# Optimization experiments

Measured on AMD Instinct MI355X. Metric: run time of the kernel, lower is better.

The kernel has to match this reference:

```python
import jax, jax.numpy as jnp
import numpy as np
from jax import lax

B, TZ, TT = 16, 2048, 512
D, DFF, L, V, HEADS = 256, 1024, 6, 512, 4
CH, HID, K, FLOWS, G = 256, 256, 5, 4, 256
PAD_ID = 0
NEG = -1e9
SCALE = 0.02


def setup_inputs():
    key = jax.random.key(0)
    ks = jax.random.split(key, 20)
    n = lambda i, shape, s=SCALE: jax.random.normal(ks[i], shape, jnp.float32) * s
    return {
        'z': jax.random.normal(ks[0], (B, TZ, CH), jnp.float32),
        'text': jax.random.randint(ks[1], (B, TT), 1, V),  # low=1 so no pad tokens
        'cond': jax.random.normal(ks[2], (B, G), jnp.float32),
        'embed': n(3, (V, D), 1.0),
        'wq': n(4, (L, D, D)), 'wk': n(5, (L, D, D)), 'wv': n(6, (L, D, D)), 'wo': n(7, (L, D, D)),
        'bq': jnp.zeros((L, D)), 'bk': jnp.zeros((L, D)), 'bv': jnp.zeros((L, D)), 'bo': jnp.zeros((L, D)),
        'ln1_g': jnp.ones((L, D)), 'ln1_b': jnp.zeros((L, D)),
        'ln2_g': jnp.ones((L, D)), 'ln2_b': jnp.zeros((L, D)),
        'w1': n(8, (L, D, DFF)), 'b1': jnp.zeros((L, DFF)),
        'w2': n(9, (L, DFF, D)), 'b2': jnp.zeros((L, D)),
        'mu_w': n(10, (D, D)), 'mu_b': jnp.zeros((D,)),
        'lv_w': n(11, (D, D)), 'lv_b': jnp.zeros((D,)),
        'flow_in': n(12, (FLOWS, CH // 2, HID)), 'flow_in_b': jnp.zeros((FLOWS, HID)),
        'flow_cond': n(13, (FLOWS, G, HID)),
        'flow_conv': n(14, (FLOWS, K, HID, HID)), 'flow_conv_b': jnp.zeros((FLOWS, HID)),
        'flow_out': n(15, (FLOWS, HID, CH // 2)), 'flow_out_b': jnp.zeros((FLOWS, CH // 2)),
    }


def _pos_encoding(length, d):
    pos = np.arange(length)[:, None].astype(np.float32)
    i = np.arange(d)[None, :]
    angle = pos / np.power(10000.0, (2 * (i // 2)) / d)
    pe = np.where(i % 2 == 0, np.sin(angle), np.cos(angle))
    return jnp.asarray(pe, jnp.float32)


def _ln(x, g, b):
    m = jnp.mean(x, -1, keepdims=True)
    v = jnp.var(x, -1, keepdims=True)
    return g * (x - m) * lax.rsqrt(v + 1e-6) + b


def _mha(x, wq, wk, wv, wo, bq, bk, bv, bo, bias):
    Bq, T, _ = x.shape
    dh = D // HEADS
    heads = lambda y: y.reshape(Bq, T, HEADS, dh).transpose(0, 2, 1, 3)
    q, k, v = heads(x @ wq + bq), heads(x @ wk + bk), heads(x @ wv + bv)
    scores = jnp.einsum('bhqd,bhkd->bhqk', q, k) / jnp.sqrt(jnp.float32(dh)) + bias
    attn = jax.nn.softmax(scores, axis=-1)
    out = jnp.einsum('bhqk,bhkd->bhqd', attn, v).transpose(0, 2, 1, 3).reshape(Bq, T, D)
    return out @ wo + bo


def _mas_path(logp, text_mask):
    # Viterbi monotonic alignment: each latent frame t maps to text index j(t),
    # j nondecreasing with steps in {0, 1}, start at 0, end at last valid token.
    Bq, Tz, Tt = logp.shape
    Q0 = jnp.where(jnp.arange(Tt) == 0, logp[:, 0, :], NEG)

    def fwd(Q, lt):
        Qs = jnp.concatenate([jnp.full((Bq, 1), NEG, Q.dtype), Q[:, :-1]], axis=1)
        return lt + jnp.maximum(Q, Qs), Qs > Q  # choice True => came from j-1

    _, choices = lax.scan(fwd, Q0, jnp.swapaxes(logp, 0, 1)[1:])  # [Tz-1,B,Tt]
    j_last = jnp.sum(text_mask, axis=1).astype(jnp.int32) - 1

    def bwd(j, ch):
        c = jnp.take_along_axis(ch, j[:, None], axis=1)[:, 0]
        jp = j - c.astype(jnp.int32)
        return jp, jp

    _, path_rev = lax.scan(bwd, j_last, choices[::-1])
    path = jnp.concatenate([path_rev[::-1], j_last[None]], axis=0)  # [Tz,B]
    return jnp.swapaxes(path, 0, 1)


def _forward(z, text, cond, embed, wq, wk, wv, wo, bq, bk, bv, bo, ln1_g, ln1_b, ln2_g, ln2_b,
             w1, b1, w2, b2, mu_w, mu_b, lv_w, lv_b,
             flow_in, flow_in_b, flow_cond, flow_conv, flow_conv_b, flow_out, flow_out_b):
    text_mask = text != PAD_ID  # [B,TT]
    bias = jnp.where(text_mask[:, None, None, :], 0.0, NEG)
    # text encoder: scaled embedding + sinusoidal PE + post-LN transformer blocks
    h = embed[text] * jnp.sqrt(jnp.float32(D)) + _pos_encoding(TT, D)[None]
    for l in range(L):
        h = _ln(h + _mha(h, wq[l], wk[l], wv[l], wo[l], bq[l], bk[l], bv[l], bo[l], bias), ln1_g[l], ln1_b[l])
        ffn = jax.nn.relu(h @ w1[l] + b1[l]) @ w2[l] + b2[l]
        h = _ln(h + ffn, ln2_g[l], ln2_b[l])
    mu = h @ mu_w + mu_b
    logvar = h @ lv_w + lv_b
    # residual coupling flows (mean-only, conditioned on global vector)
    zc = z
    for f in range(FLOWS):
        x0, x1 = jnp.split(zc, 2, axis=-1)
        hh = x0 @ flow_in[f] + flow_in_b[f] + (cond @ flow_cond[f])[:, None, :]
        hh = jnp.tanh(lax.conv_general_dilated(hh, flow_conv[f], (1,), 'SAME', rhs_dilation=(1,),
                                               dimension_numbers=('NWC', 'WIO', 'NWC')) + flow_conv_b[f])
        m = hh @ flow_out[f] + flow_out_b[f]
        zc = jnp.concatenate([x1 + m, x0], axis=-1)  # coupling + flip
    # gaussian log-likelihood between latent frames and text distributions
    spr = jnp.exp(-logvar)  # [B,TT,D]
    nc1 = jnp.sum(-0.5 * jnp.log(2.0 * jnp.pi) - 0.5 * logvar, axis=-1)  # [B,TT]
    nc2 = jnp.einsum('btd,bjd->btj', -0.5 * zc * zc, spr)
    nc3 = jnp.einsum('btd,bjd->btj', zc, mu * spr)
    nc4 = jnp.sum(-0.5 * mu * mu * spr, axis=-1)  # [B,TT]
    logp = nc1[:, None, :] + nc2 + nc3 + nc4[:, None, :]  # [B,TZ,TT]
    logp = jnp.where(text_mask[:, None, :], logp, NEG)
    path = _mas_path(logp, text_mask)  # [B,TZ] int32
    ctx = mu[jnp.arange(B)[:, None], path]  # expand text mu along latent time
    return ctx, h


def reference(z, text, cond, embed, wq, wk, wv, wo, bq, bk, bv, bo, ln1_g, ln1_b, ln2_g, ln2_b,
              w1, b1, w2, b2, mu_w, mu_b, lv_w, lv_b,
              flow_in, flow_in_b, flow_cond, flow_conv, flow_conv_b, flow_out, flow_out_b):
    return _forward(z, text, cond, embed, wq, wk, wv, wo, bq, bk, bv, bo, ln1_g, ln1_b, ln2_g, ln2_b,
                    w1, b1, w2, b2, mu_w, mu_b, lv_w, lv_b,
                    flow_in, flow_in_b, flow_cond, flow_conv, flow_conv_b, flow_out, flow_out_b)
```

## Files before the change

kernel.cpp:

```cpp
#include <hip/hip_runtime.h>

#define BB 16
#define TZ_ 2048
#define TT_ 512
#define D_ 256
#define DFF_ 1024
#define L_ 6
#define HEADS_ 4
#define DH_ 64
#define CH_ 256
#define HID_ 256
#define KCV 5
#define FLOWS_ 4
#define G_ 256
#define NEGF (-1000000000.0f)
#define LOG2PI 1.8378770664093453f

typedef unsigned short u16;
typedef __attribute__((ext_vector_type(8))) short short8v;
typedef __attribute__((ext_vector_type(4))) float f32x4;
typedef __attribute__((ext_vector_type(4))) unsigned u4v;

__device__ __forceinline__ float wsum(float v){
#pragma unroll
  for (int o = 32; o; o >>= 1) v += __shfl_xor(v, o);
  return v;
}
__device__ __forceinline__ u16 f2bf(float x){
  unsigned u = __float_as_uint(x);
  return (u16)((u + 0x7FFFu + ((u >> 16) & 1u)) >> 16);
}
__device__ __forceinline__ float bf2f(u16 h){
  return __uint_as_float(((unsigned)h) << 16);
}
__device__ __forceinline__ unsigned pk2f(float a, float b){
  return __builtin_amdgcn_perm(__float_as_uint(b), __float_as_uint(a), 0x07060302u);
}
__device__ __forceinline__ float trnc(float f){
  return __uint_as_float(__float_as_uint(f) & 0xFFFF0000u);
}
__device__ __forceinline__ void cvt8t(float4 x, float4 y, uint4 &hi, uint4 &lo){
  hi.x = pk2f(x.x, x.y); hi.y = pk2f(x.z, x.w);
  hi.z = pk2f(y.x, y.y); hi.w = pk2f(y.z, y.w);
  float r0 = x.x - trnc(x.x), r1 = x.y - trnc(x.y), r2 = x.z - trnc(x.z), r3 = x.w - trnc(x.w);
  float r4 = y.x - trnc(y.x), r5 = y.y - trnc(y.y), r6 = y.z - trnc(y.z), r7 = y.w - trnc(y.w);
  lo.x = pk2f(r0, r1); lo.y = pk2f(r2, r3); lo.z = pk2f(r4, r5); lo.w = pk2f(r6, r7);
}
__device__ __forceinline__ unsigned rneh(float f){
  unsigned v = __float_as_uint(f);
  return (v + 0x7FFFu + ((v >> 16) & 1u)) & 0xFFFF0000u;
}
__device__ __forceinline__ void cvt8r(float4 x, float4 y, uint4 &hi, uint4 &lo){
  unsigned h0=rneh(x.x), h1=rneh(x.y), h2=rneh(x.z), h3=rneh(x.w);
  unsigned h4=rneh(y.x), h5=rneh(y.y), h6=rneh(y.z), h7=rneh(y.w);
  hi.x = h1 | (h0>>16); hi.y = h3 | (h2>>16); hi.z = h5 | (h4>>16); hi.w = h7 | (h6>>16);
  float r0 = x.x - __uint_as_float(h0), r1 = x.y - __uint_as_float(h1);
  float r2 = x.z - __uint_as_float(h2), r3 = x.w - __uint_as_float(h3);
  float r4 = y.x - __uint_as_float(h4), r5 = y.y - __uint_as_float(h5);
  float r6 = y.z - __uint_as_float(h6), r7 = y.w - __uint_as_float(h7);
  lo.x = pk2f(r0, r1); lo.y = pk2f(r2, r3); lo.z = pk2f(r4, r5); lo.w = pk2f(r6, r7);
}

__global__ void k_pe(float* __restrict__ pe){
  int t = blockIdx.x, d = threadIdx.x;
  double e = (double)(2*(d>>1)) / (double)D_;
  double ang = (double)t * pow(10000.0, -e);
  pe[t*D_ + d] = (float)(((d&1)==0) ? sin(ang) : cos(ang));
}
__global__ void k_embed(const int* __restrict__ text, const float* __restrict__ emb,
                        const float* __restrict__ pe, float* __restrict__ h){
  int row = blockIdx.x, d = threadIdx.x;
  h[(size_t)row*D_ + d] = emb[(size_t)text[row]*D_ + d]*16.0f + pe[(row%TT_)*D_ + d];
}

__global__ __launch_bounds__(256) void k_wt(
  const float* __restrict__ wq, const float* __restrict__ wk,
  const float* __restrict__ wv, const float* __restrict__ wo,
  const float* __restrict__ mu_w, const float* __restrict__ lv_w,
  const float* __restrict__ w1, const float* __restrict__ w2,
  float* __restrict__ QKVT, float* __restrict__ OT, float* __restrict__ MULVT,
  float* __restrict__ W1T, float* __restrict__ W2T)
{
  __shared__ float td[64][65];
  const int s = blockIdx.y, tile = blockIdx.x, t = threadIdx.x;
  const float* inb; float* outb; int istride, ostride;
  if (s < 24){
    int l = s>>2, wsel = s&3;
    const float* w = (wsel==0?wq:wsel==1?wk:wsel==2?wv:wo);
    inb = w + (size_t)l*65536; istride = 256;
    if (wsel < 3) outb = QKVT + (size_t)l*196608 + wsel*65536;
    else          outb = OT   + (size_t)l*65536;
    ostride = 256;
  } else if (s < 26){
    inb = (s==24 ? mu_w : lv_w); istride = 256;
    outb = MULVT + (size_t)(s-24)*65536; ostride = 256;
  } else if (s < 50){
    int idx = s-26, l = idx>>2, b2 = idx&3;
    inb = w1 + (size_t)l*262144 + b2*256; istride = 1024;
    outb = W1T + (size_t)l*262144 + (size_t)b2*65536; ostride = 256;
  } else {
    int idx = s-50, l = idx>>2, b2 = idx&3;
    inb = w2 + (size_t)l*262144 + (size_t)b2*65536; istride = 256;
    outb = W2T + (size_t)l*262144 + b2*256; ostride = 1024;
  }
  const int kt = (tile>>2)*64, nt = (tile&3)*64;
  const int r = t>>2, cq = (t&3)*16;
#pragma unroll
  for (int c=0;c<16;c+=4){
    float4 v = *(const float4*)(inb + (size_t)(kt + r)*istride + nt + cq + c);
    td[r][cq+c+0]=v.x; td[r][cq+c+1]=v.y; td[r][cq+c+2]=v.z; td[r][cq+c+3]=v.w;
  }
  __syncthreads();
#pragma unroll
  for (int c=0;c<16;c+=4){
    float4 v = make_float4(td[cq+c+0][r], td[cq+c+1][r], td[cq+c+2][r], td[cq+c+3][r]);
    *(float4*)(outb + (size_t)(nt + r)*ostride + kt + cq + c) = v;
  }
}

__global__ __launch_bounds__(256) void k_vt(const float* __restrict__ QKV, float* __restrict__ VT){
  __shared__ float td[64][65];
  const int b = blockIdx.z, dt = blockIdx.x, jt = blockIdx.y, t = threadIdx.x;
  const float* inb = QKV + (size_t)b*512*768 + 512;
  float* outb = VT + (size_t)b*131072;
  const int r = t>>2, cq = (t&3)*16;
#pragma unroll
  for (int c=0;c<16;c+=4){
    float4 v = *(const float4*)(inb + (size_t)(jt*64 + r)*768 + dt*64 + cq + c);
    td[r][cq+c+0]=v.x; td[r][cq+c+1]=v.y; td[r][cq+c+2]=v.z; td[r][cq+c+3]=v.w;
  }
  __syncthreads();
#pragma unroll
  for (int c=0;c<16;c+=4){
    float4 v = make_float4(td[cq+c+0][r], td[cq+c+1][r], td[cq+c+2][r], td[cq+c+3][r]);
    *(float4*)(outb + (size_t)(dt*64 + r)*512 + jt*64 + cq + c) = v;
  }
}

__global__ void k_bcat(const float* __restrict__ bq, const float* __restrict__ bk,
                       const float* __restrict__ bv, const float* __restrict__ mu_b,
                       const float* __restrict__ lv_b,
                       float* __restrict__ BQKV, float* __restrict__ MULVB){
  int i = blockIdx.x*256 + threadIdx.x;
  if (i < 4608){
    int l = i/768, c = i%768;
    float v = c<256 ? bq[l*256+c] : (c<512 ? bk[l*256+c-256] : bv[l*256+c-512]);
    BQKV[i] = v;
  } else if (i < 5120){
    int c = i-4608;
    MULVB[c] = c<256 ? mu_b[c] : lv_b[c-256];
  }
}

template<int WN, int EPI, int AM, int BMD>
__global__ __launch_bounds__(256,2) void k_mg(
  const void* __restrict__ Ap, const void* __restrict__ ApL, int lda, int azhi, int azlo,
  const void* __restrict__ Bp, const void* __restrict__ BpL, int ldb, int bzhi, int bzlo,
  const float* __restrict__ bias, const int* __restrict__ text,
  const float* __restrict__ nc1v, const float* __restrict__ nc4v,
  float* __restrict__ C, int ldc, int czhi, int czlo, int K)
{
  constexpr int BN = WN*32;
  __shared__ u16 AH[4096], AL[4096];
  __shared__ u16 BH[BN*32], BL[BN*32];
  char* AHB=(char*)AH; char* ALB=(char*)AL; char* BHB=(char*)BH; char* BLB=(char*)BL;
  const int t = threadIdx.x, z = blockIdx.z;
  const int m0 = blockIdx.y*128, n0 = blockIdx.x*BN;
  const size_t aoff = (size_t)(z>>2)*azhi + (size_t)(z&3)*azlo;
  const size_t boff = (size_t)(z>>2)*bzhi + (size_t)(z&3)*bzlo;
  const size_t coff = (size_t)(z>>2)*czhi + (size_t)(z&3)*czlo;
  const int w = t>>6, l = t&63;
  const int wr = (w>>1)*64, wc = (w&1)*(WN*16);
  const int lr = l&15, lg = l>>4;
  const int srow = t>>1, sseg = t&1;
  const int q  = (srow>>1)&3;
  const int wo0 = srow*64 + ((((sseg<<1)|0)^q)<<4);
  const int wo1 = srow*64 + ((((sseg<<1)|1)^q)<<4);
  const bool bact = (WN==4) || (t < 128);
  const int qa = ((wr+lr)>>1)&3, qb2 = ((wc+lr)>>1)&3;
  const int raBase = (wr+lr)*64 + ((lg^qa)<<4);
  const int rbBase = (wc+lr)*64 + ((lg^qb2)<<4);

  const float* Af = nullptr; const u16* AfH = nullptr; const u16* AfL = nullptr;
  if constexpr (AM==0 || AM==2 || AM==4){ Af = (const float*)Ap + aoff; }
  else { AfH = (const u16*)Ap + aoff; AfL = (const u16*)ApL + aoff; }
  const float* Bf = nullptr; const u16* BfH = nullptr; const u16* BfL = nullptr;
  if constexpr (BMD==0){ Bf = (const float*)Bp + boff; }
  else { BfH = (const u16*)Bp + boff; BfL = (const u16*)BpL + boff; }

  float mrow = 0.f, sinv = 0.f;
  if constexpr (AM==4){
    int rg = z*TT_ + m0 + srow;
    mrow = nc1v[rg];
    sinv = nc4v[rg];
  }

  float4 sa0, sa1, sa2, sa3;
  uint4  pah0, pah1, pal0, pal1;
  float4 sb0, sb1, sb2, sb3;
  uint4  pbh0, pbh1, pbl0, pbl1;

  auto LOADA = [&](int kk){
    if constexpr (AM==0 || AM==4){
      const float* p = Af + (size_t)(m0+srow)*lda + kk + sseg*16;
      sa0=*(const float4*)p; sa1=*(const float4*)(p+4);
      sa2=*(const float4*)(p+8); sa3=*(const float4*)(p+12);
    } else if constexpr (AM==1){
      const u16* ph = AfH + (size_t)(m0+srow)*lda + kk + sseg*16;
      const u16* pl = AfL + (size_t)(m0+srow)*lda + kk + sseg*16;
      pah0 = *(const uint4*)ph; pah1 = *(const uint4*)(ph+8);
      pal0 = *(const uint4*)pl; pal1 = *(const uint4*)(pl+8);
    } else {
      int kg = kk + sseg*16;
      const float* p = Af + (size_t)(m0+srow)*lda + (kg < 256 ? kg : kg - 256);
      sa0=*(const float4*)p; sa1=*(const float4*)(p+4);
      sa2=*(const float4*)(p+8); sa3=*(const float4*)(p+12);
    }
  };
  auto LOADB = [&](int kk){
    if constexpr (BMD==0){
      const float* p = Bf + (size_t)(n0+srow)*ldb + kk + sseg*16;
      sb0=*(const float4*)p; sb1=*(const float4*)(p+4);
      sb2=*(const float4*)(p+8); sb3=*(const float4*)(p+12);
    } else {
      const u16* ph = BfH + (size_t)(n0+srow)*ldb + kk + sseg*16;
      const u16* pl = BfL + (size_t)(n0+srow)*ldb + kk + sseg*16;
      pbh0 = *(const uint4*)ph; pbh1 = *(const uint4*)(ph+8);
      pbl0 = *(const uint4*)pl; pbl1 = *(const uint4*)(pl+8);
    }
  };
  auto WRITEA = [&](int kk){
    uint4 ahi0, ahi1, alo0, alo1;
    if constexpr (AM==0){
      cvt8t(sa0,sa1,ahi0,alo0); cvt8t(sa2,sa3,ahi1,alo1);
    } else if constexpr (AM==4){
      float4 a0=sa0, a1=sa1, a2=sa2, a3=sa3;
      a0.x=expf(a0.x-mrow)*sinv; a0.y=expf(a0.y-mrow)*sinv; a0.z=expf(a0.z-mrow)*sinv; a0.w=expf(a0.w-mrow)*sinv;
      a1.x=expf(a1.x-mrow)*sinv; a1.y=expf(a1.y-mrow)*sinv; a1.z=expf(a1.z-mrow)*sinv; a1.w=expf(a1.w-mrow)*sinv;
      a2.x=expf(a2.x-mrow)*sinv; a2.y=expf(a2.y-mrow)*sinv; a2.z=expf(a2.z-mrow)*sinv; a2.w=expf(a2.w-mrow)*sinv;
      a3.x=expf(a3.x-mrow)*sinv; a3.y=expf(a3.y-mrow)*sinv; a3.z=expf(a3.z-mrow)*sinv; a3.w=expf(a3.w-mrow)*sinv;
      cvt8t(a0,a1,ahi0,alo0); cvt8t(a2,a3,ahi1,alo1);
    } else if constexpr (AM==1){
      ahi0=pah0; ahi1=pah1; alo0=pal0; alo1=pal1;
    } else {
      float4 a0=sa0, a1=sa1, a2=sa2, a3=sa3;
      int kg = kk + sseg*16;
      if (kg >= 256){
        a0.x=-0.5f*a0.x*a0.x; a0.y=-0.5f*a0.y*a0.y; a0.z=-0.5f*a0.z*a0.z; a0.w=-0.5f*a0.w*a0.w;
        a1.x=-0.5f*a1.x*a1.x; a1.y=-0.5f*a1.y*a1.y; a1.z=-0.5f*a1.z*a1.z; a1.w=-0.5f*a1.w*a1.w;
        a2.x=-0.5f*a2.x*a2.x; a2.y=-0.5f*a2.y*a2.y; a2.z=-0.5f*a2.z*a2.z; a2.w=-0.5f*a2.w*a2.w;
        a3.x=-0.5f*a3.x*a3.x; a3.y=-0.5f*a3.y*a3.y; a3.z=-0.5f*a3.z*a3.z; a3.w=-0.5f*a3.w*a3.w;
      }
      cvt8r(a0,a1,ahi0,alo0); cvt8r(a2,a3,ahi1,alo1);
    }
    *(uint4*)(AHB + wo0) = ahi0;  *(uint4*)(AHB + wo1) = ahi1;
    *(uint4*)(ALB + wo0) = alo0;  *(uint4*)(ALB + wo1) = alo1;
  };
  auto WRITEB = [&](){
    uint4 bhi0, bhi1, blo0, blo1;
    if constexpr (BMD==0){
      cvt8t(sb0,sb1,bhi0,blo0); cvt8t(sb2,sb3,bhi1,blo1);
    } else {
      bhi0=pbh0; bhi1=pbh1; blo0=pbl0; blo1=pbl1;
    }
    *(uint4*)(BHB + wo0) = bhi0;  *(uint4*)(BHB + wo1) = bhi1;
    *(uint4*)(BLB + wo0) = blo0;  *(uint4*)(BLB + wo1) = blo1;
  };

  f32x4 acc[4][WN];
#pragma unroll
  for (int i=0;i<4;i++)
#pragma unroll
    for (int j=0;j<WN;j++) acc[i][j] = (f32x4){0.f,0.f,0.f,0.f};

  LOADA(0);
  if (bact) LOADB(0);
  for (int k0 = 0; k0 < K; k0 += 32){
    __syncthreads();
    WRITEA(k0);
    if (bact) WRITEB();
    if (k0 + 32 < K){ LOADA(k0+32); if (bact) LOADB(k0+32); }
    __syncthreads();
    short8v fah[4], fal[4], fbh[WN], fbl[WN];
#pragma unroll
    for (int i=0;i<4;i++){
      fah[i] = *(short8v*)(AHB + raBase + i*1024);
      fal[i] = *(short8v*)(ALB + raBase + i*1024);
    }
#pragma unroll
    for (int j=0;j<WN;j++){
      fbh[j] = *(short8v*)(BHB + rbBase + j*1024);
      fbl[j] = *(short8v*)(BLB + rbBase + j*1024);
    }
#pragma unroll
    for (int i=0;i<4;i++)
#pragma unroll
      for (int j=0;j<WN;j++){
        acc[i][j] = __builtin_amdgcn_mfma_f32_16x16x32_bf16(fah[i], fbh[j], acc[i][j], 0,0,0);
        acc[i][j] = __builtin_amdgcn_mfma_f32_16x16x32_bf16(fal[i], fbh[j], acc[i][j], 0,0,0);
        acc[i][j] = __builtin_amdgcn_mfma_f32_16x16x32_bf16(fah[i], fbl[j], acc[i][j], 0,0,0);
      }
  }

#pragma unroll
  for (int i=0;i<4;i++){
    int mm0 = m0 + wr + i*16 + (lg<<2);
#pragma unroll
    for (int j=0;j<WN;j++){
      int nn = n0 + wc + j*16 + lr;
      float bs = 0.f; float ncb = 0.f; bool msk = true;
      if (EPI==0 || EPI==1) bs = bias ? bias[nn] : 0.f;
      if (EPI==2) msk = (text[(z>>2)*TT_ + nn] != 0);
      if (EPI==3){ ncb = nc1v[z*TT_+nn] + nc4v[z*TT_+nn]; msk = (text[z*TT_+nn] != 0); }
      f32x4 v = acc[i][j];
#pragma unroll
      for (int r=0;r<4;r++){
        int m = mm0 + r;
        float x;
        if (EPI==0)      x = v[r] + bs;
        else if (EPI==1) x = fmaxf(v[r] + bs, 0.f);
        else if (EPI==2) x = v[r]*0.125f + (msk ? 0.f : NEGF);
        else             x = msk ? (v[r] + ncb) : NEGF;
        C[coff + (size_t)m*ldc + nn] = x;
      }
    }
  }
}

__global__ __launch_bounds__(256) void k_rowstat(const float* __restrict__ S,
  float* __restrict__ MR, float* __restrict__ SR){
  size_t row = (size_t)blockIdx.x*4 + (threadIdx.x >> 6);
  const float* p = S + row*TT_;
  int ln = threadIdx.x & 63;
  float4 a = *(const float4*)(p + ln*8);
  float4 b = *(const float4*)(p + ln*8 + 4);
  float x[8] = {a.x,a.y,a.z,a.w,b.x,b.y,b.z,b.w};
  float m = x[0];
#pragma unroll
  for (int i=1;i<8;i++) m = fmaxf(m, x[i]);
#pragma unroll
  for (int o2=32;o2;o2>>=1) m = fmaxf(m, __shfl_xor(m, o2));
  float s = 0.f;
#pragma unroll
  for (int i=0;i<8;i++){ s += expf(x[i]-m); }
  s = wsum(s);
  if (ln == 0){
    MR[row] = m;
    SR[row] = 1.0f/s;
  }
}

__global__ __launch_bounds__(256) void k_lnres(const float* __restrict__ y,
  const float* __restrict__ g, const float* __restrict__ bb, float* __restrict__ h){
  size_t row = blockIdx.x; int d = threadIdx.x;
  float v = h[row*D_ + d] + y[row*D_ + d];
  float s = wsum(v), s2 = wsum(v*v);
  __shared__ float r1[4], r2[4];
  int w = d >> 6;
  if ((d & 63) == 0){ r1[w] = s; r2[w] = s2; }
  __syncthreads();
  s  = r1[0]+r1[1]+r1[2]+r1[3];
  s2 = r2[0]+r2[1]+r2[2]+r2[3];
  float mean = s * (1.0f/D_);
  float var  = s2 * (1.0f/D_) - mean*mean;
  float inv  = rsqrtf(var + 1e-6f);
  h[row*D_ + d] = g[d]*(v - mean)*inv + bb[d];
}

__global__ __launch_bounds__(256) void k_prep(const float* __restrict__ mulv,
  u16* __restrict__ b2h, u16* __restrict__ b2l,
  float* __restrict__ nc1, float* __restrict__ nc4){
  size_t row = blockIdx.x; int d = threadIdx.x;
  float m = mulv[row*512 + d];
  float lv = mulv[row*512 + 256 + d];
  float sp = expf(-lv);
  float ms = m*sp;
  float s1 = wsum(lv), s2 = wsum(m*ms);
  __shared__ float r1[4], r2[4];
  int w = d >> 6;
  if ((d&63)==0){ r1[w]=s1; r2[w]=s2; }
  __syncthreads();
  if (d == 0){
    nc1[row] = -0.5f*((float)D_*LOG2PI + (r1[0]+r1[1]+r1[2]+r1[3]));
    nc4[row] = -0.5f*(r2[0]+r2[1]+r2[2]+r2[3]);
  }
  unsigned hm = rneh(ms);
  b2h[row*512 + d] = (u16)(hm>>16);
  b2l[row*512 + d] = f2bf(ms - __uint_as_float(hm));
  unsigned hs = rneh(sp);
  b2h[row*512 + 256 + d] = (u16)(hs>>16);
  b2l[row*512 + 256 + d] = f2bf(sp - __uint_as_float(hs));
}

__global__ __launch_bounds__(256) void k_fprep(
  const float* __restrict__ win, const float* __restrict__ wconv, const float* __restrict__ wout,
  u16* __restrict__ WITH, u16* __restrict__ WITL,
  u16* __restrict__ WCTH, u16* __restrict__ WCTL,
  u16* __restrict__ WOTH, u16* __restrict__ WOTL,
  const float* __restrict__ zsrc, u16* __restrict__ xh, u16* __restrict__ xl,
  const float* __restrict__ cond, const float* __restrict__ fcw, float* __restrict__ condp)
{
  const int bid = blockIdx.x, t = threadIdx.x;
  if (bid < 1536){
    int i = bid*256 + t;
    float wv2; u16 *dh, *dl; int idx;
    if (i < 32768){
      int n = i >> 7, k = i & 127;
      wv2 = win[k*256 + n]; dh = WITH; dl = WITL; idx = i;
    } else if (i < 360448){
      int jj = i - 32768;
      int o = jj / 1280, r = jj - o*1280;
      wv2 = wconv[(size_t)r*256 + o]; dh = WCTH; dl = WCTL; idx = jj;
    } else {
      int jj = i - 360448;
      int o = jj >> 8, k = jj & 255;
      wv2 = wout[k*128 + o]; dh = WOTH; dl = WOTL; idx = jj;
    }
    u16 hh = f2bf(wv2);
    dh[idx] = hh;
    dl[idx] = f2bf(wv2 - bf2f(hh));
  } else if (bid < 3584){
    size_t i = ((size_t)(bid-1536)*256 + t) << 3;
    size_t m2 = i >> 7; int k = (int)(i & 127);
    const float* src = zsrc + m2*256 + k;
    float4 a = *(const float4*)src; float4 b2 = *(const float4*)(src+4);
    float vv[8] = {a.x,a.y,a.z,a.w,b2.x,b2.y,b2.z,b2.w};
    short8v oh, ol;
#pragma unroll
    for (int r=0;r<8;r++){
      u16 hh = f2bf(vv[r]);
      oh[r] = (short)hh;
      ol[r] = (short)f2bf(vv[r] - bf2f(hh));
    }
    *(short8v*)(xh + i) = oh;
    *(short8v*)(xl + i) = ol;
  } else {
    int b = bid - 3584, n = t;
    float s = 0.f;
    for (int k2=0;k2<G_;k2++) s = fmaf(cond[b*G_ + k2], fcw[k2*HID_ + n], s);
    condp[b*HID_ + n] = s;
  }
}

__global__ void k_padzero2(u16* __restrict__ XpH, u16* __restrict__ XpL){
  int i = blockIdx.x*256 + threadIdx.x;
  u16* P = (i >> 14) ? XpL : XpH;
  int ii = i & 16383;
  int b = ii >> 10, rr = (ii >> 8) & 3, c = ii & 255;
  int row = (rr < 2) ? rr : (2048 + rr);
  P[((size_t)b*2052 + row)*256 + c] = 0;
}

template<int EPI, int SPLITOUT>
__global__ __launch_bounds__(256,2) void k_mf2(
  const u16* __restrict__ Ah, const u16* __restrict__ Al, int lda, int padA,
  const u16* __restrict__ Bh, const u16* __restrict__ Bl, int ldb,
  const float* __restrict__ bias, const float* __restrict__ cnd,
  void* __restrict__ CH, void* __restrict__ CL, int ldc, int padC, int K)
{
  __shared__ u16 AsmH[4096], AsmL[4096], BsmH[4096], BsmL[4096];
  char* AHB=(char*)AsmH; char* ALB=(char*)AsmL;
  char* BHB=(char*)BsmH; char* BLB=(char*)BsmL;
  const int t = threadIdx.x;
  const int m0 = blockIdx.y << 7, n0 = blockIdx.x << 7;
  const int w = t >> 6, l = t & 63;
  const int wr = (w >> 1) << 6, wc = (w & 1) << 6;
  const int lr = l & 15, lg = l >> 4;
  const int srow = t >> 1, sseg = t & 1;
  const int q = (srow >> 1) & 3;
  const int wo0 = srow*64 + ((((sseg<<1)|0) ^ q) << 4);
  const int wo1 = srow*64 + ((((sseg<<1)|1) ^ q) << 4);
  const int am = m0 + srow;
  const size_t aoff = (size_t)(am + padA*(am >> 11))*lda + (sseg << 4);
  const u16* AhP = Ah + aoff;
  const u16* AlP = Al + aoff;
  const size_t boff = (size_t)(n0 + srow)*ldb + (sseg << 4);
  const u16* BhP = Bh + boff;
  const u16* BlP = Bl + boff;
  const int qa = ((wr + lr) >> 1) & 3, qb = ((wc + lr) >> 1) & 3;
  const int raBase = (wr + lr)*64 + ((lg ^ qa) << 4);
  const int rbBase = (wc + lr)*64 + ((lg ^ qb) << 4);
  f32x4 acc[4][4];
#pragma unroll
  for (int i=0;i<4;i++)
#pragma unroll
    for (int j=0;j<4;j++) acc[i][j] = (f32x4){0.f,0.f,0.f,0.f};

  float4 sah0, sah1, sal0, sal1, sbh0, sbh1, sbl0, sbl1;
  auto LOADF = [&](int kk){
    sah0 = *(const float4*)(AhP + kk); sah1 = *(const float4*)(AhP + kk + 8);
    sal0 = *(const float4*)(AlP + kk); sal1 = *(const float4*)(AlP + kk + 8);
    sbh0 = *(const float4*)(BhP + kk); sbh1 = *(const float4*)(BhP + kk + 8);
    sbl0 = *(const float4*)(BlP + kk); sbl1 = *(const float4*)(BlP + kk + 8);
  };

  LOADF(0);
  for (int k0 = 0; k0 < K; k0 += 32){
    __syncthreads();
    *(float4*)(AHB + wo0) = sah0;  *(float4*)(AHB + wo1) = sah1;
    *(float4*)(ALB + wo0) = sal0;  *(float4*)(ALB + wo1) = sal1;
    *(float4*)(BHB + wo0) = sbh0;  *(float4*)(BHB + wo1) = sbh1;
    *(float4*)(BLB + wo0) = sbl0;  *(float4*)(BLB + wo1) = sbl1;
    if (k0 + 32 < K) LOADF(k0 + 32);
    __syncthreads();
    short8v fah[4], fal[4], fbh[4], fbl[4];
#pragma unroll
    for (int i=0;i<4;i++){
      fah[i] = *(short8v*)(AHB + raBase + i*1024);
      fal[i] = *(short8v*)(ALB + raBase + i*1024);
    }
#pragma unroll
    for (int j=0;j<4;j++){
      fbh[j] = *(short8v*)(BHB + rbBase + j*1024);
      fbl[j] = *(short8v*)(BLB + rbBase + j*1024);
    }
#pragma unroll
    for (int i=0;i<4;i++)
#pragma unroll
      for (int j=0;j<4;j++){
        acc[i][j] = __builtin_amdgcn_mfma_f32_16x16x32_bf16(fah[i], fbh[j], acc[i][j], 0, 0, 0);
        acc[i][j] = __builtin_amdgcn_mfma_f32_16x16x32_bf16(fal[i], fbh[j], acc[i][j], 0, 0, 0);
        acc[i][j] = __builtin_amdgcn_mfma_f32_16x16x32_bf16(fah[i], fbl[j], acc[i][j], 0, 0, 0);
      }
  }

#pragma unroll
  for (int i=0;i<4;i++){
    int mbase = m0 + wr + i*16 + (lg << 2);
#pragma unroll
    for (int j=0;j<4;j++){
      int nn = n0 + wc + j*16 + lr;
      float bs = bias[nn];
      f32x4 v = acc[i][j];
#pragma unroll
      for (int r=0;r<4;r++){
        int m = mbase + r;
        float x = v[r] + bs;
        if (EPI == 1) x += cnd[((m >> 11) << 8) + nn];
        if (EPI == 2) x = tanhf(x);
        if (EPI == 3) x += cnd[(size_t)m*256 + 128 + nn];
        size_t ro = (size_t)(m + padC*(m >> 11))*ldc + nn;
        if (SPLITOUT){
          u16 xh = f2bf(x);
          ((u16*)CH)[ro] = xh;
          ((u16*)CL)[ro] = f2bf(x - bf2f(xh));
        } else {
          ((float*)CH)[ro] = x;
          if (EPI == 3)
            ((float*)CH)[(size_t)m*ldc + 128 + nn] = cnd[(size_t)m*256 + nn];
        }
      }
    }
  }
}

__device__ __forceinline__ void mas_row1(float4 u0, float4 u1, float* Q, int ln, int tr,
                                         unsigned char* __restrict__ cb){
  float v[8] = {u0.x,u0.y,u0.z,u0.w,u1.x,u1.y,u1.z,u1.w};
  float qp = __shfl_up(Q[7], 1);
  if (ln == 0) qp = NEGF;
  unsigned bits = 0; float qs = qp;
#pragma unroll
  for (int i=0;i<8;i++){
    float old = Q[i];
    if (qs > old) bits |= (1u<<i);
    Q[i] = v[i] + fmaxf(old, qs);
    qs = old;
  }
  cb[(size_t)(tr-1)*64 + ln] = (unsigned char)bits;
}

__global__ __launch_bounds__(64,1) void k_mas(const float* __restrict__ lp,
  const int* __restrict__ text, unsigned char* __restrict__ cho, int* __restrict__ path)
{
  const int b = blockIdx.x, ln = threadIdx.x;
  const float* L = lp + (size_t)b*TZ_*TT_;
  const float* Lr = L + ln*8;
  unsigned char* cb = cho + (size_t)b*TZ_*64;
  __shared__ __align__(16) unsigned char lch[3*4096];

  float Q[8];
#pragma unroll
  for (int i=0;i<8;i++) Q[i] = NEGF;
  if (ln == 0) Q[0] = L[0];

  float4 P0a = *(const float4*)(Lr + (size_t)1*TT_), P0b = *(const float4*)(Lr + (size_t)1*TT_ + 4);
  float4 P1a = *(const float4*)(Lr + (size_t)2*TT_), P1b = *(const float4*)(Lr + (size_t)2*TT_ + 4);
  float4 P2a = *(const float4*)(Lr + (size_t)3*TT_), P2b = *(const float4*)(Lr + (size_t)3*TT_ + 4);
  float4 P3a = *(const float4*)(Lr + (size_t)4*TT_), P3b = *(const float4*)(Lr + (size_t)4*TT_ + 4);
  float4 P4a = *(const float4*)(Lr + (size_t)5*TT_), P4b = *(const float4*)(Lr + (size_t)5*TT_ + 4);
  float4 P5a = *(const float4*)(Lr + (size_t)6*TT_), P5b = *(const float4*)(Lr + (size_t)6*TT_ + 4);
  float4 P6a = *(const float4*)(Lr + (size_t)7*TT_), P6b = *(const float4*)(Lr + (size_t)7*TT_ + 4);
  float4 P7a = *(const float4*)(Lr + (size_t)8*TT_), P7b = *(const float4*)(Lr + (size_t)8*TT_ + 4);
  asm volatile("" ::: "memory");

  int t0 = 1;
#define MAS_SLOT(Pa, Pb, OFF) \
    mas_row1(Pa, Pb, Q, ln, t0 + OFF, cb); \
    { const float* _s = Lr + (size_t)(t0 + OFF + 8)*TT_; \
      Pa = *(const float4*)_s; Pb = *(const float4*)(_s + 4); } \
    asm volatile("" ::: "memory");
  for (; t0 + 15 <= TZ_ - 1; t0 += 8){
    MAS_SLOT(P0a, P0b, 0)
    MAS_SLOT(P1a, P1b, 1)
    MAS_SLOT(P2a, P2b, 2)
    MAS_SLOT(P3a, P3b, 3)
    MAS_SLOT(P4a, P4b, 4)
    MAS_SLOT(P5a, P5b, 5)
    MAS_SLOT(P6a, P6b, 6)
    MAS_SLOT(P7a, P7b, 7)
  }
#undef MAS_SLOT
  mas_row1(P0a,P0b,Q,ln,t0+0,cb);
  mas_row1(P1a,P1b,Q,ln,t0+1,cb);
  mas_row1(P2a,P2b,Q,ln,t0+2,cb);
  mas_row1(P3a,P3b,Q,ln,t0+3,cb);
  mas_row1(P4a,P4b,Q,ln,t0+4,cb);
  mas_row1(P5a,P5b,Q,ln,t0+5,cb);
  mas_row1(P6a,P6b,Q,ln,t0+6,cb);
  mas_row1(P7a,P7b,Q,ln,t0+7,cb);
  for (int t = t0 + 8; t < TZ_; t++){
    const float* s = Lr + (size_t)t*TT_;
    float4 a = *(const float4*)s;
    float4 c = *(const float4*)(s + 4);
    mas_row1(a, c, Q, ln, t, cb);
  }

  int cnt = 0;
#pragma unroll
  for (int i=0;i<8;i++) cnt += (text[b*TT_ + ln*8 + i] != 0) ? 1 : 0;
#pragma unroll
  for (int o2=32;o2;o2>>=1) cnt += __shfl_xor(cnt, o2);
  const int jl = cnt - 1;
  if (ln == 0) path[b*TZ_ + TZ_-1] = jl;

  __syncthreads();

  const int NP = TZ_ - 1;
  uint* lchU = (uint*)lch;
  const uint* cbU = (const uint*)cb;
  {
    int r0 = 2046 - ln;
#pragma unroll
    for (int k=0;k<4;k++)
      *(u4v*)&lchU[0*1024 + ln*16 + k*4] = *(const u4v*)&cbU[(size_t)r0*16 + k*4];
    int r1 = 2046 - (64 + ln);
#pragma unroll
    for (int k=0;k<4;k++)
      *(u4v*)&lchU[1*1024 + ln*16 + k*4] = *(const u4v*)&cbU[(size_t)r1*16 + k*4];
  }
  u4v su0, su1, su2, su3;
  {
    int r2 = 2046 - (128 + ln);
    su0 = *(const u4v*)&cbU[(size_t)r2*16 + 0];
    su1 = *(const u4v*)&cbU[(size_t)r2*16 + 4];
    su2 = *(const u4v*)&cbU[(size_t)r2*16 + 8];
    su3 = *(const u4v*)&cbU[(size_t)r2*16 + 12];
  }

  int j = jl;
  unsigned rb0[8], rb1[8]; int rc[8];
  if (ln == 0){
#pragma unroll
    for (int qd=0; qd<8; qd++){
      int cHi = jl >> 3;
      int cLo = (cHi > 0) ? cHi - 1 : 0;
      rb1[qd] = lch[qd*64 + cHi];
      rb0[qd] = lch[qd*64 + cLo];
      rc[qd]  = cHi;
    }
  }
  for (int H = 0; H < 32; H++){
    if (H + 2 < 32){
      uint* wb = lchU + ((H+2)%3)*1024;
      *(u4v*)&wb[ln*16 + 0]  = su0;
      *(u4v*)&wb[ln*16 + 4]  = su1;
      *(u4v*)&wb[ln*16 + 8]  = su2;
      *(u4v*)&wb[ln*16 + 12] = su3;
    }
    if (H + 3 < 32){
      int p = (H+3)*64 + ln;
      if (p <= 2046){
        int r = 2046 - p;
        su0 = *(const u4v*)&cbU[(size_t)r*16 + 0];
        su1 = *(const u4v*)&cbU[(size_t)r*16 + 4];
        su2 = *(const u4v*)&cbU[(size_t)r*16 + 8];
        su3 = *(const u4v*)&cbU[(size_t)r*16 + 12];
      }
    }
    if (ln == 0){
      int pbase = H*64;
#pragma unroll 8
      for (int s = 0; s < 64; s++){
        int p = pbase + s;
        if (p < NP){
          int r = s & 7;
          int jb = j >> 3;
          unsigned byte = (jb == rc[r]) ? rb1[r] : rb0[r];
          j -= (int)((byte >> (j & 7)) & 1u);
          path[b*TZ_ + 2046 - p] = j;
          int pn = p + 8;
          if (pn < NP){
            int hn = (pn >> 6) % 3, sn = pn & 63;
            int cHi = j >> 3;
            int cLo = (cHi > 0) ? cHi - 1 : 0;
            rb1[r] = lch[hn*4096 + sn*64 + cHi];
            rb0[r] = lch[hn*4096 + sn*64 + cLo];
            rc[r]  = cHi;
          }
        }
      }
    }
    __syncthreads();
  }
}

__global__ void k_gather(const float* __restrict__ mulv, const int* __restrict__ path,
  const float* __restrict__ h, float* __restrict__ out){
  size_t i = (size_t)blockIdx.x*256 + threadIdx.x;
  const size_t N4 = (size_t)BB*TZ_*(D_/4);
  const size_t H4 = (size_t)BB*TT_*(D_/4);
  if (i < N4){
    size_t row = i >> 6; int c = (int)(i & 63);
    int b = (int)(row >> 11);
    int pj = path[row];
    ((float4*)out)[i] = *(const float4*)(mulv + ((size_t)b*TT_ + pj)*512 + (size_t)c*4);
  } else if (i < N4 + H4){
    size_t k2 = i - N4;
    ((float4*)out)[i] = ((const float4*)h)[k2];
  }
}

extern "C" void kernel_launch(void* const* d_in, const int* in_sizes, int n_in,
                              void* d_out, int out_size, void* d_ws, size_t ws_size,
                              hipStream_t stream)
{
  (void)in_sizes; (void)n_in; (void)out_size; (void)ws_size;
  const float* z      = (const float*)d_in[0];
  const int*   text   = (const int*)  d_in[1];
  const float* cond   = (const float*)d_in[2];
  const float* emb    = (const float*)d_in[3];
  const float* wq     = (const float*)d_in[4];
  const float* wk     = (const float*)d_in[5];
  const float* wv     = (const float*)d_in[6];
  const float* wo     = (const float*)d_in[7];
  const float* bq     = (const float*)d_in[8];
  const float* bk     = (const float*)d_in[9];
  const float* bv     = (const float*)d_in[10];
  const float* bo     = (const float*)d_in[11];
  const float* ln1g   = (const float*)d_in[12];
  const float* ln1b   = (const float*)d_in[13];
  const float* ln2g   = (const float*)d_in[14];
  const float* ln2b   = (const float*)d_in[15];
  const float* w1     = (const float*)d_in[16];
  const float* b1     = (const float*)d_in[17];
  const float* w2     = (const float*)d_in[18];
  const float* b2     = (const float*)d_in[19];
  const float* mu_w   = (const float*)d_in[20];
  const float* mu_b   = (const float*)d_in[21];
  const float* lv_w   = (const float*)d_in[22];
  const float* lv_b   = (const float*)d_in[23];
  const float* f_in   = (const float*)d_in[24];
  const float* f_in_b = (const float*)d_in[25];
  const float* f_cond = (const float*)d_in[26];
  const float* f_conv = (const float*)d_in[27];
  const float* f_convb= (const float*)d_in[28];
  const float* f_out  = (const float*)d_in[29];
  const float* f_outb = (const float*)d_in[30];

  float* ws = (float*)d_ws;
  size_t o = 0;
  float* PE   = ws + o; o += (size_t)131072;
  float* H    = ws + o; o += (size_t)2097152;
  float* MULV = ws + o; o += (size_t)4194304;
  float* NC1  = ws + o; o += (size_t)8192;
  float* NC4  = ws + o; o += (size_t)8192;
  float* MR   = ws + o; o += (size_t)32768;
  float* SR   = ws + o; o += (size_t)32768;
  float* CONDP= ws + o; o += (size_t)4096;
  int*   PATH = (int*)(ws + o); o += (size_t)32768;
  u16*  B2H  = (u16*)(ws + o); o += (size_t)2097152;
  u16*  B2L  = (u16*)(ws + o); o += (size_t)2097152;
  float* BIGS = ws + o; o += (size_t)16777216;
  float* BUF1 = ws + o; o += (size_t)4587520;
  float* BUF2 = ws + o; o += (size_t)10485760;
  float* ZCA  = ws + o; o += (size_t)8388608;
  float* ZCB  = ws + o; o += (size_t)8388608;

  float* QKV = BUF2;
  float* Yb  = QKV + 6291456;
  float* VT  = Yb + 2097152;
  float* ATTO= QKV;
  float* QKVT = ZCA;
  float* OT   = QKVT + 1179648;
  float* W1T  = OT + 393216;
  float* W2T  = W1T + 1572864;
  float* MULVT= W2T + 1572864;
  float* BQKV = MULVT + 131072;
  float* MULVB= BQKV + 4608;
  u16*  X0H = (u16*)BUF1;
  u16*  X0L = X0H + 4194304;
  u16*  WITH = X0L + 4194304;
  u16*  WITL = WITH + 32768;
  u16*  WCTH = WITL + 32768;
  u16*  WCTL = WCTH + 327680;
  u16*  WOTH = WCTL + 327680;
  u16*  WOTL = WOTH + 32768;
  u16*  XpH = (u16*)BIGS;
  u16*  XpL = XpH + 8404992;
  u16*  H2H = (u16*)BUF2;
  u16*  H2L = H2H + 8388608;
  unsigned char* CHO = (unsigned char*)ZCA;

  k_pe   <<<dim3(TT_),    dim3(D_), 0, stream>>>(PE);
  k_embed<<<dim3(BB*TT_), dim3(D_), 0, stream>>>(text, emb, PE, H);
  k_wt   <<<dim3(16,74), 256, 0, stream>>>(wq,wk,wv,wo,mu_w,lv_w,w1,w2, QKVT,OT,MULVT,W1T,W2T);
  k_bcat <<<dim3(20), 256, 0, stream>>>(bq,bk,bv,mu_b,lv_b, BQKV, MULVB);

  for (int l=0;l<L_;l++){
    k_mg<4,0,0,0><<<dim3(6,64,1),256,0,stream>>>(
      H, nullptr, 256, 0,0,  QKVT + (size_t)l*196608, nullptr, 256, 0,0,
      BQKV + l*768, nullptr, nullptr, nullptr, QKV, 768, 0,0, 256);
    k_vt <<<dim3(4,8,16),256,0,stream>>>(QKV, VT);
    k_mg<4,2,0,0><<<dim3(4,4,64),256,0,stream>>>(
      QKV, nullptr, 768, 393216, 64,  QKV+256, nullptr, 768, 393216, 64,
      nullptr, text, nullptr, nullptr, BIGS, 512, 1048576, 262144, 64);
    k_rowstat<<<dim3(BB*HEADS_*TT_/4),256,0,stream>>>(BIGS, MR, SR);
    k_mg<2,0,4,0><<<dim3(1,4,64),256,0,stream>>>(
      BIGS, nullptr, 512, 1048576, 262144,  VT, nullptr, 512, 131072, 32768,
      nullptr, nullptr, MR, SR, Yb, 256, 131072, 64, 512);
    k_mg<4,0,0,0><<<dim3(2,64,1),256,0,stream>>>(
      Yb, nullptr, 256, 0,0,  OT + (size_t)l*65536, nullptr, 256, 0,0,
      bo + l*256, nullptr, nullptr, nullptr, ATTO, 256, 0,0, 256);
    k_lnres<<<dim3(BB*TT_),256,0,stream>>>(ATTO, ln1g+l*D_, ln1b+l*D_, H);
    k_mg<4,1,0,0><<<dim3(8,64,1),256,0,stream>>>(
      H, nullptr, 256, 0,0,  W1T + (size_t)l*262144, nullptr, 256, 0,0,
      b1 + l*1024, nullptr, nullptr, nullptr, BIGS, 1024, 0,0, 256);
    k_mg<4,0,0,0><<<dim3(2,64,1),256,0,stream>>>(
      BIGS, nullptr, 1024, 0,0,  W2T + (size_t)l*262144, nullptr, 1024, 0,0,
      b2 + l*256, nullptr, nullptr, nullptr, ATTO, 256, 0,0, 1024);
    k_lnres<<<dim3(BB*TT_),256,0,stream>>>(ATTO, ln2g+l*D_, ln2b+l*D_, H);
  }

  k_mg<4,0,0,0><<<dim3(4,64,1),256,0,stream>>>(
    H, nullptr, 256, 0,0,  MULVT, nullptr, 256, 0,0,
    MULVB, nullptr, nullptr, nullptr, MULV, 512, 0,0, 256);
  k_prep<<<dim3(BB*TT_),256,0,stream>>>(MULV, B2H, B2L, NC1, NC4);

  k_padzero2<<<dim3(128),256,0,stream>>>(XpH, XpL);
  const float* zsrc = z;
  for (int f=0; f<FLOWS_; f++){
    k_fprep<<<dim3(3600),256,0,stream>>>(
        f_in + (size_t)f*(CH_/2)*HID_, f_conv + (size_t)f*KCV*HID_*HID_,
        f_out + (size_t)f*HID_*(CH_/2),
        WITH, WITL, WCTH, WCTL, WOTH, WOTL,
        zsrc, X0H, X0L,
        cond, f_cond + (size_t)f*G_*HID_, CONDP);
    k_mf2<1,1><<<dim3(2,256),256,0,stream>>>(X0H, X0L, 128, 0, WITH, WITL, 128,
        f_in_b + f*HID_, CONDP, (void*)(XpH + 512), (void*)(XpL + 512), 256, 4, 128);
    k_mf2<2,1><<<dim3(2,256),256,0,stream>>>(XpH, XpL, 256, 4, WCTH, WCTL, 1280,
        f_convb + f*HID_, nullptr, (void*)H2H, (void*)H2L, 256, 0, 1280);
    float* zdst = (f & 1) ? ZCB : ZCA;
    k_mf2<3,0><<<dim3(1,256),256,0,stream>>>(H2H, H2L, 256, 0, WOTH, WOTL, 256,
        f_outb + f*(CH_/2), zsrc, (void*)zdst, nullptr, 256, 0, 256);
    zsrc = zdst;
  }

  k_mg<4,3,2,1><<<dim3(4,16,16),256,0,stream>>>(
    zsrc, nullptr, 256, 2097152, 524288,
    B2H, B2L, 512, 1048576, 262144,
    nullptr, text, NC1, NC4, BIGS, 512, 4194304, 1048576, 512);

  k_mas<<<dim3(BB),64,0,stream>>>(BIGS, text, CHO, PATH);
  k_gather<<<dim3((BB*TZ_*D_/4 + BB*TT_*D_/4)/256),256,0,stream>>>(MULV, PATH, H, (float*)d_out);
}
```

Baseline: 2.157 ms.

## Stream MAS logp rows into an LDS ring buffer via async global-to-LDS loads

The serial MAS forward pass now prefetches logp rows 24 ahead into a 32-row shared-memory ring buffer using global_load_lds, instead of holding eight rows of prefetch in registers. It waits with explicit vmcnt counters and then reads each row from LDS. The aim is to hide global memory latency in this single-wave, latency-bound loop with a much deeper prefetch. In exchange it uses 64KB of LDS and relies on hand-tuned waitcnt values. Wrong counts or the lack of LDS visibility ordering for the async writes could cause races.

```diff
diff --git a/kernel.cpp b/kernel.cpp
--- a/kernel.cpp
+++ b/kernel.cpp
@@ -575,8 +575,8 @@
 {
   const int b = blockIdx.x, ln = threadIdx.x;
   const float* L = lp + (size_t)b*TZ_*TT_;
-  const float* Lr = L + ln*8;
   unsigned char* cb = cho + (size_t)b*TZ_*64;
+  __shared__ float ring[32*TT_];
   __shared__ __align__(16) unsigned char lch[3*4096];
 
   float Q[8];
@@ -584,43 +584,38 @@
   for (int i=0;i<8;i++) Q[i] = NEGF;
   if (ln == 0) Q[0] = L[0];
 
-  float4 P0a = *(const float4*)(Lr + (size_t)1*TT_), P0b = *(const float4*)(Lr + (size_t)1*TT_ + 4);
-  float4 P1a = *(const float4*)(Lr + (size_t)2*TT_), P1b = *(const float4*)(Lr + (size_t)2*TT_ + 4);
-  float4 P2a = *(const float4*)(Lr + (size_t)3*TT_), P2b = *(const float4*)(Lr + (size_t)3*TT_ + 4);
-  float4 P3a = *(const float4*)(Lr + (size_t)4*TT_), P3b = *(const float4*)(Lr + (size_t)4*TT_ + 4);
-  float4 P4a = *(const float4*)(Lr + (size_t)5*TT_), P4b = *(const float4*)(Lr + (size_t)5*TT_ + 4);
-  float4 P5a = *(const float4*)(Lr + (size_t)6*TT_), P5b = *(const float4*)(Lr + (size_t)6*TT_ + 4);
-  float4 P6a = *(const float4*)(Lr + (size_t)7*TT_), P6b = *(const float4*)(Lr + (size_t)7*TT_ + 4);
-  float4 P7a = *(const float4*)(Lr + (size_t)8*TT_), P7b = *(const float4*)(Lr + (size_t)8*TT_ + 4);
-  asm volatile("" ::: "memory");
-
-  int t0 = 1;
-#define MAS_SLOT(Pa, Pb, OFF) \
-    mas_row1(Pa, Pb, Q, ln, t0 + OFF, cb); \
-    { const float* _s = Lr + (size_t)(t0 + OFF + 8)*TT_; \
-      Pa = *(const float4*)_s; Pb = *(const float4*)(_s + 4); } \
+#define GL2(ROW) { \
+    const float* _g0 = L + (size_t)(ROW)*TT_ + ln*4; \
+    __builtin_amdgcn_global_load_lds( \
+      (const __attribute__((address_space(1))) void*)_g0, \
+      (__attribute__((address_space(3))) void*)&ring[((ROW)&31)*TT_], 16, 0, 0); \
+    const float* _g1 = _g0 + 256; \
+    __builtin_amdgcn_global_load_lds( \
+      (const __attribute__((address_space(1))) void*)_g1, \
+      (__attribute__((address_space(3))) void*)&ring[((ROW)&31)*TT_ + 256], 16, 0, 0); }
+
+  for (int r = 1; r <= 24; r++) GL2(r)
+  for (int p = 1; p <= 2025; p += 8){
+    asm volatile("s_waitcnt vmcnt(32)" ::: "memory");
+#pragma unroll
+    for (int k = 0; k < 8; k++){
+      int t = p + k;
+      const float* s = &ring[(t & 31)*TT_ + ln*8];
+      float4 a = *(const float4*)s;
+      float4 c = *(const float4*)(s + 4);
+      mas_row1(a, c, Q, ln, t, cb);
+    }
     asm volatile("" ::: "memory");
-  for (; t0 + 15 <= TZ_ - 1; t0 += 8){
-    MAS_SLOT(P0a, P0b, 0)
-    MAS_SLOT(P1a, P1b, 1)
-    MAS_SLOT(P2a, P2b, 2)
-    MAS_SLOT(P3a, P3b, 3)
-    MAS_SLOT(P4a, P4b, 4)
-    MAS_SLOT(P5a, P5b, 5)
-    MAS_SLOT(P6a, P6b, 6)
-    MAS_SLOT(P7a, P7b, 7)
-  }
-#undef MAS_SLOT
-  mas_row1(P0a,P0b,Q,ln,t0+0,cb);
-  mas_row1(P1a,P1b,Q,ln,t0+1,cb);
-  mas_row1(P2a,P2b,Q,ln,t0+2,cb);
-  mas_row1(P3a,P3b,Q,ln,t0+3,cb);
-  mas_row1(P4a,P4b,Q,ln,t0+4,cb);
-  mas_row1(P5a,P5b,Q,ln,t0+5,cb);
-  mas_row1(P6a,P6b,Q,ln,t0+6,cb);
-  mas_row1(P7a,P7b,Q,ln,t0+7,cb);
-  for (int t = t0 + 8; t < TZ_; t++){
-    const float* s = Lr + (size_t)t*TT_;
+#pragma unroll
+    for (int k = 0; k < 8; k++){
+      int r = p + 24 + k;
+      if (r < TZ_) GL2(r)
+    }
+  }
+#undef GL2
+  asm volatile("s_waitcnt vmcnt(0)" ::: "memory");
+  for (int t = 2033; t < TZ_; t++){
+    const float* s = &ring[(t & 31)*TT_ + ln*8];
     float4 a = *(const float4*)s;
     float4 c = *(const float4*)(s + 4);
     mas_row1(a, c, Q, ln, t, cb);
```

Measured after the change: 2.307 ms. 1.07x slower.

## Add a prefetch helper wave to warm cache ahead of the MAS forward scan

Applied to the files above, without the earlier changes.

Doubles the MAS block to two waves. The first wave runs the sequential forward DP as before and publishes its row progress to a shared variable. The second wave reads the log-prob rows ahead of it, bounded by a fixed window, so they sit in cache when the DP wave arrives. The goal is to hide global-memory latency in the serial scan. The cost is a spin-wait on a volatile shared variable, extra memory traffic, and a second wave that competes for issue slots.

```diff
diff --git a/kernel.cpp b/kernel.cpp
--- a/kernel.cpp
+++ b/kernel.cpp
@@ -570,76 +570,101 @@
   cb[(size_t)(tr-1)*64 + ln] = (unsigned char)bits;
 }
 
-__global__ __launch_bounds__(64,1) void k_mas(const float* __restrict__ lp,
+__global__ __launch_bounds__(128,1) void k_mas(const float* __restrict__ lp,
   const int* __restrict__ text, unsigned char* __restrict__ cho, int* __restrict__ path)
 {
-  const int b = blockIdx.x, ln = threadIdx.x;
+  const int b = blockIdx.x, t = threadIdx.x, ln = t & 63;
   const float* L = lp + (size_t)b*TZ_*TT_;
   const float* Lr = L + ln*8;
   unsigned char* cb = cho + (size_t)b*TZ_*64;
   __shared__ __align__(16) unsigned char lch[3*4096];
-
-  float Q[8];
-#pragma unroll
-  for (int i=0;i<8;i++) Q[i] = NEGF;
-  if (ln == 0) Q[0] = L[0];
-
-  float4 P0a = *(const float4*)(Lr + (size_t)1*TT_), P0b = *(const float4*)(Lr + (size_t)1*TT_ + 4);
-  float4 P1a = *(const float4*)(Lr + (size_t)2*TT_), P1b = *(const float4*)(Lr + (size_t)2*TT_ + 4);
-  float4 P2a = *(const float4*)(Lr + (size_t)3*TT_), P2b = *(const float4*)(Lr + (size_t)3*TT_ + 4);
-  float4 P3a = *(const float4*)(Lr + (size_t)4*TT_), P3b = *(const float4*)(Lr + (size_t)4*TT_ + 4);
-  float4 P4a = *(const float4*)(Lr + (size_t)5*TT_), P4b = *(const float4*)(Lr + (size_t)5*TT_ + 4);
-  float4 P5a = *(const float4*)(Lr + (size_t)6*TT_), P5b = *(const float4*)(Lr + (size_t)6*TT_ + 4);
-  float4 P6a = *(const float4*)(Lr + (size_t)7*TT_), P6b = *(const float4*)(Lr + (size_t)7*TT_ + 4);
-  float4 P7a = *(const float4*)(Lr + (size_t)8*TT_), P7b = *(const float4*)(Lr + (size_t)8*TT_ + 4);
-  asm volatile("" ::: "memory");
-
-  int t0 = 1;
+  __shared__ int prog;
+  if (t == 0) prog = 0;
+  __syncthreads();
+
+  int jl = 0;
+  if (t < 64){
+    float Q[8];
+#pragma unroll
+    for (int i=0;i<8;i++) Q[i] = NEGF;
+    if (ln == 0) Q[0] = L[0];
+
+    float4 P0a = *(const float4*)(Lr + (size_t)1*TT_), P0b = *(const float4*)(Lr + (size_t)1*TT_ + 4);
+    float4 P1a = *(const float4*)(Lr + (size_t)2*TT_), P1b = *(const float4*)(Lr + (size_t)2*TT_ + 4);
+    float4 P2a = *(const float4*)(Lr + (size_t)3*TT_), P2b = *(const float4*)(Lr + (size_t)3*TT_ + 4);
+    float4 P3a = *(const float4*)(Lr + (size_t)4*TT_), P3b = *(const float4*)(Lr + (size_t)4*TT_ + 4);
+    float4 P4a = *(const float4*)(Lr + (size_t)5*TT_), P4b = *(const float4*)(Lr + (size_t)5*TT_ + 4);
+    float4 P5a = *(const float4*)(Lr + (size_t)6*TT_), P5b = *(const float4*)(Lr + (size_t)6*TT_ + 4);
+    float4 P6a = *(const float4*)(Lr + (size_t)7*TT_), P6b = *(const float4*)(Lr + (size_t)7*TT_ + 4);
+    float4 P7a = *(const float4*)(Lr + (size_t)8*TT_), P7b = *(const float4*)(Lr + (size_t)8*TT_ + 4);
+    asm volatile("" ::: "memory");
+
+    int t0 = 1;
 #define MAS_SLOT(Pa, Pb, OFF) \
-    mas_row1(Pa, Pb, Q, ln, t0 + OFF, cb); \
-    { const float* _s = Lr + (size_t)(t0 + OFF + 8)*TT_; \
-      Pa = *(const float4*)_s; Pb = *(const float4*)(_s + 4); } \
-    asm volatile("" ::: "memory");
-  for (; t0 + 15 <= TZ_ - 1; t0 += 8){
-    MAS_SLOT(P0a, P0b, 0)
-    MAS_SLOT(P1a, P1b, 1)
-    MAS_SLOT(P2a, P2b, 2)
-    MAS_SLOT(P3a, P3b, 3)
-    MAS_SLOT(P4a, P4b, 4)
-    MAS_SLOT(P5a, P5b, 5)
-    MAS_SLOT(P6a, P6b, 6)
-    MAS_SLOT(P7a, P7b, 7)
-  }
+      mas_row1(Pa, Pb, Q, ln, t0 + OFF, cb); \
+      { const float* _s = Lr + (size_t)(t0 + OFF + 8)*TT_; \
+        Pa = *(const float4*)_s; Pb = *(const float4*)(_s + 4); } \
+      asm volatile("" ::: "memory");
+    for (; t0 + 15 <= TZ_ - 1; t0 += 8){
+      if (ln == 0) *((volatile int*)&prog) = t0;
+      MAS_SLOT(P0a, P0b, 0)
+      MAS_SLOT(P1a, P1b, 1)
+      MAS_SLOT(P2a, P2b, 2)
+      MAS_SLOT(P3a, P3b, 3)
+      MAS_SLOT(P4a, P4b, 4)
+      MAS_SLOT(P5a, P5b, 5)
+      MAS_SLOT(P6a, P6b, 6)
+      MAS_SLOT(P7a, P7b, 7)
+    }
 #undef MAS_SLOT
-  mas_row1(P0a,P0b,Q,ln,t0+0,cb);
-  mas_row1(P1a,P1b,Q,ln,t0+1,cb);
-  mas_row1(P2a,P2b,Q,ln,t0+2,cb);
-  mas_row1(P3a,P3b,Q,ln,t0+3,cb);
-  mas_row1(P4a,P4b,Q,ln,t0+4,cb);
-  mas_row1(P5a,P5b,Q,ln,t0+5,cb);
-  mas_row1(P6a,P6b,Q,ln,t0+6,cb);
-  mas_row1(P7a,P7b,Q,ln,t0+7,cb);
-  for (int t = t0 + 8; t < TZ_; t++){
-    const float* s = Lr + (size_t)t*TT_;
-    float4 a = *(const float4*)s;
-    float4 c = *(const float4*)(s + 4);
-    mas_row1(a, c, Q, ln, t, cb);
-  }
-
-  int cnt = 0;
-#pragma unroll
-  for (int i=0;i<8;i++) cnt += (text[b*TT_ + ln*8 + i] != 0) ? 1 : 0;
-#pragma unroll
-  for (int o2=32;o2;o2>>=1) cnt += __shfl_xor(cnt, o2);
-  const int jl = cnt - 1;
-  if (ln == 0) path[b*TZ_ + TZ_-1] = jl;
+    mas_row1(P0a,P0b,Q,ln,t0+0,cb);
+    mas_row1(P1a,P1b,Q,ln,t0+1,cb);
+    mas_row1(P2a,P2b,Q,ln,t0+2,cb);
+    mas_row1(P3a,P3b,Q,ln,t0+3,cb);
+    mas_row1(P4a,P4b,Q,ln,t0+4,cb);
+    mas_row1(P5a,P5b,Q,ln,t0+5,cb);
+    mas_row1(P6a,P6b,Q,ln,t0+6,cb);
+    mas_row1(P7a,P7b,Q,ln,t0+7,cb);
+    for (int tt = t0 + 8; tt < TZ_; tt++){
+      const float* s = Lr + (size_t)tt*TT_;
+      float4 a = *(const float4*)s;
+      float4 c = *(const float4*)(s + 4);
+      mas_row1(a, c, Q, ln, tt, cb);
+    }
+
+    int cnt = 0;
+#pragma unroll
+    for (int i=0;i<8;i++) cnt += (text[b*TT_ + ln*8 + i] != 0) ? 1 : 0;
+#pragma unroll
+    for (int o2=32;o2;o2>>=1) cnt += __shfl_xor(cnt, o2);
+    jl = cnt - 1;
+    if (ln == 0){
+      path[b*TZ_ + TZ_-1] = jl;
+      *((volatile int*)&prog) = (int)TZ_;
+    }
+  } else {
+    volatile int* vp = &prog;
+    float acc = 0.f;
+    for (int r = 9; r < TZ_; r += 2){
+      while (r - *vp > 160) { }
+      const float* s0 = L + (size_t)r*TT_ + ln*8;
+      float4 a = *(const float4*)s0;
+      float4 c = *(const float4*)(s0 + 4);
+      const float* s1 = s0 + TT_;
+      float4 d0 = *(const float4*)s1;
+      float4 e0 = *(const float4*)(s1 + 4);
+      acc += a.x+a.y+a.z+a.w + c.x+c.y+c.z+c.w;
+      acc += d0.x+d0.y+d0.z+d0.w + e0.x+e0.y+e0.z+e0.w;
+    }
+    asm volatile("" :: "v"(acc));
+  }
 
   __syncthreads();
 
   const int NP = TZ_ - 1;
   uint* lchU = (uint*)lch;
   const uint* cbU = (const uint*)cb;
-  {
+  if (t < 64){
     int r0 = 2046 - ln;
 #pragma unroll
     for (int k=0;k<4;k++)
@@ -650,7 +675,7 @@
       *(u4v*)&lchU[1*1024 + ln*16 + k*4] = *(const u4v*)&cbU[(size_t)r1*16 + k*4];
   }
   u4v su0, su1, su2, su3;
-  {
+  if (t < 64){
     int r2 = 2046 - (128 + ln);
     su0 = *(const u4v*)&cbU[(size_t)r2*16 + 0];
     su1 = *(const u4v*)&cbU[(size_t)r2*16 + 4];
@@ -660,7 +685,7 @@
 
   int j = jl;
   unsigned rb0[8], rb1[8]; int rc[8];
-  if (ln == 0){
+  if (t == 0){
 #pragma unroll
     for (int qd=0; qd<8; qd++){
       int cHi = jl >> 3;
@@ -671,24 +696,26 @@
     }
   }
   for (int H = 0; H < 32; H++){
-    if (H + 2 < 32){
-      uint* wb = lchU + ((H+2)%3)*1024;
-      *(u4v*)&wb[ln*16 + 0]  = su0;
-      *(u4v*)&wb[ln*16 + 4]  = su1;
-      *(u4v*)&wb[ln*16 + 8]  = su2;
-      *(u4v*)&wb[ln*16 + 12] = su3;
-    }
-    if (H + 3 < 32){
-      int p = (H+3)*64 + ln;
-      if (p <= 2046){
-        int r = 2046 - p;
-        su0 = *(const u4v*)&cbU[(size_t)r*16 + 0];
-        su1 = *(const u4v*)&cbU[(size_t)r*16 + 4];
-        su2 = *(const u4v*)&cbU[(size_t)r*16 + 8];
-        su3 = *(const u4v*)&cbU[(size_t)r*16 + 12];
+    if (t < 64){
+      if (H + 2 < 32){
+        uint* wb = lchU + ((H+2)%3)*1024;
+        *(u4v*)&wb[ln*16 + 0]  = su0;
+        *(u4v*)&wb[ln*16 + 4]  = su1;
+        *(u4v*)&wb[ln*16 + 8]  = su2;
+        *(u4v*)&wb[ln*16 + 12] = su3;
       }
-    }
-    if (ln == 0){
+      if (H + 3 < 32){
+        int p = (H+3)*64 + ln;
+        if (p <= 2046){
+          int r = 2046 - p;
+          su0 = *(const u4v*)&cbU[(size_t)r*16 + 0];
+          su1 = *(const u4v*)&cbU[(size_t)r*16 + 4];
+          su2 = *(const u4v*)&cbU[(size_t)r*16 + 8];
+          su3 = *(const u4v*)&cbU[(size_t)r*16 + 12];
+        }
+      }
+    }
+    if (t == 0){
       int pbase = H*64;
 #pragma unroll 8
       for (int s = 0; s < 64; s++){
@@ -871,6 +898,6 @@
     B2H, B2L, 512, 1048576, 262144,
     nullptr, text, NC1, NC4, BIGS, 512, 4194304, 1048576, 512);
 
-  k_mas<<<dim3(BB),64,0,stream>>>(BIGS, text, CHO, PATH);
+  k_mas<<<dim3(BB),128,0,stream>>>(BIGS, text, CHO, PATH);
   k_gather<<<dim3((BB*TZ_*D_/4 + BB*TT_*D_/4)/256),256,0,stream>>>(MULV, PATH, H, (float*)d_out);
 }
```

Result: slower. 2.229 ms (+3.3%).
